# Kernel optimization log

Hardware: AMD Instinct MI355X
Metric: run time of the kernel (lower is better)

## Reference

```python
import jax, jax.numpy as jnp
import numpy as np

NUM_GRAPHS = 512

def _add_self_loops(edge_index, n):
    loop = jnp.arange(n, dtype=edge_index.dtype)
    src = jnp.concatenate([edge_index[0], loop])
    dst = jnp.concatenate([edge_index[1], loop])
    return src, dst

def _segment_softmax(e, seg, n):
    m = jax.ops.segment_max(e, seg, num_segments=n)
    e = jnp.exp(e - m[seg])
    s = jax.ops.segment_sum(e, seg, num_segments=n)
    return e / (s[seg] + 1e-16)

def _gat_conv(x, edge_index, W, a_src, a_dst, b, heads, ch):
    n = x.shape[0]
    src, dst = _add_self_loops(edge_index, n)
    h = (x @ W).reshape(n, heads, ch)                      # [N,H,C]
    al = (h * a_src).sum(-1)                               # [N,H]
    ar = (h * a_dst).sum(-1)                               # [N,H]
    e = jax.nn.leaky_relu(al[src] + ar[dst], 0.2)          # [E,H]
    alpha = _segment_softmax(e, dst, n)                    # [E,H]
    out = jax.ops.segment_sum(h[src] * alpha[:, :, None], dst, num_segments=n)
    return out.reshape(n, heads * ch) + b

def _gcn_conv(x, edge_index, W, b):
    n = x.shape[0]
    src, dst = _add_self_loops(edge_index, n)
    h = x @ W
    deg = jax.ops.segment_sum(jnp.ones(dst.shape, h.dtype), dst, num_segments=n)
    dis = jax.lax.rsqrt(jnp.maximum(deg, 1.0))
    norm = dis[src] * dis[dst]
    return jax.ops.segment_sum(h[src] * norm[:, None], dst, num_segments=n) + b

def _gmp(x, batch):
    return jax.ops.segment_max(x, batch, num_segments=NUM_GRAPHS)

def setup_inputs() -> dict:
    key = jax.random.key(0)
    ks = jax.random.split(key, 24)
    nd, ed = 100000, 800000
    np_, ep = 300000, 2400000
    def rn(k, shape, scale=0.1):
        return jax.random.normal(k, shape, dtype=jnp.float32) * scale
    inp = {
        "x_drug": jax.random.normal(ks[0], (nd, 78), dtype=jnp.float32),
        "edge_index_drug": jax.random.randint(ks[1], (2, ed), 0, nd, dtype=jnp.int32),
        "batch_drug": jnp.sort(jax.random.randint(ks[2], (nd,), 0, NUM_GRAPHS, dtype=jnp.int32)),
        "x_prot": jax.random.normal(ks[3], (np_, 41), dtype=jnp.float32),
        "edge_index_prot": jax.random.randint(ks[4], (2, ep), 0, np_, dtype=jnp.int32),
        "batch_prot": jnp.sort(jax.random.randint(ks[5], (np_,), 0, NUM_GRAPHS, dtype=jnp.int32)),
        # GATConv1: 78 -> 78, heads=10
        "W1": rn(ks[6], (78, 780)), "a_src1": rn(ks[7], (10, 78)), "a_dst1": rn(ks[8], (10, 78)), "b1": jnp.zeros((780,), jnp.float32),
        # GATConv2: 780 -> 128, heads=1
        "W2": rn(ks[9], (780, 128), 0.05), "a_src2": rn(ks[10], (1, 128)), "a_dst2": rn(ks[11], (1, 128)), "b2": jnp.zeros((128,), jnp.float32),
        "fc_g1_W": rn(ks[12], (128, 128)), "fc_g1_b": jnp.zeros((128,), jnp.float32),
        "gcn1_W": rn(ks[13], (41, 41)), "gcn1_b": jnp.zeros((41,), jnp.float32),
        "gcn2_W": rn(ks[14], (41, 64)), "gcn2_b": jnp.zeros((64,), jnp.float32),
        "lin1_W": rn(ks[15], (64, 128)), "lin1_b": jnp.zeros((128,), jnp.float32),
        "fc1_W": rn(ks[16], (256, 1024), 0.05), "fc1_b": jnp.zeros((1024,), jnp.float32),
        "fc2_W": rn(ks[17], (1024, 256), 0.03), "fc2_b": jnp.zeros((256,), jnp.float32),
        "out_W": rn(ks[18], (256, 1)), "out_b": jnp.zeros((1,), jnp.float32),
    }
    return inp

def reference(x_drug, edge_index_drug, batch_drug, x_prot, edge_index_prot, batch_prot,
              W1, a_src1, a_dst1, b1, W2, a_src2, a_dst2, b2, fc_g1_W, fc_g1_b,
              gcn1_W, gcn1_b, gcn2_W, gcn2_b, lin1_W, lin1_b,
              fc1_W, fc1_b, fc2_W, fc2_b, out_W, out_b):
    # drug branch (eval mode: dropout = identity)
    xd = jax.nn.elu(_gat_conv(x_drug, edge_index_drug, W1, a_src1, a_dst1, b1, 10, 78))
    xd = jax.nn.relu(_gat_conv(xd, edge_index_drug, W2, a_src2, a_dst2, b2, 1, 128))
    xd = _gmp(xd, batch_drug)
    xd = jax.nn.relu(xd @ fc_g1_W + fc_g1_b)
    # protein branch
    xp = jax.nn.relu(_gcn_conv(x_prot, edge_index_prot, gcn1_W, gcn1_b))
    xp = jax.nn.relu(_gcn_conv(xp, edge_index_prot, gcn2_W, gcn2_b))
    xp = _gmp(xp, batch_prot)
    xp = jax.nn.relu(xp @ lin1_W + lin1_b)
    # head
    xc = jnp.concatenate([xd, xp], axis=1)
    xc = jax.nn.relu(xc @ fc1_W + fc1_b)
    xc = jax.nn.relu(xc @ fc2_W + fc2_b)
    return xc @ out_W + out_b
```

## Files before the change

### kernel.cpp

```cpp
#include <hip/hip_runtime.h>
#include <math.h>

static inline int cdiv(int a, int b) { return (a + b - 1) / b; }

typedef __attribute__((ext_vector_type(8))) short short8v;
typedef __attribute__((ext_vector_type(4))) float f32x4;

__device__ inline unsigned bf16rne(float x) {
  unsigned u = __builtin_bit_cast(unsigned, x);
  return (u + 0x7FFFu + ((u >> 16) & 1u)) >> 16;
}
__device__ inline float bfhi(unsigned h) { return __builtin_bit_cast(float, h << 16); }
__device__ inline unsigned pk(float v) {
  unsigned hb = bf16rne(v);
  return hb | (bf16rne(v - bfhi(hb)) << 16);
}

__global__ void k_count(const int* __restrict__ dst, int E, int* __restrict__ cnt) {
  int i = blockIdx.x * 256 + threadIdx.x;
  if (i < E) atomicAdd(&cnt[dst[i]], 1);
}

__global__ __launch_bounds__(256) void k_scan_chunk(const int* __restrict__ in, int n,
                                                    int* __restrict__ out, int* __restrict__ sums) {
  __shared__ int tsum[256];
  int base = blockIdx.x * 1024;
  int t = threadIdx.x;
  int v[4]; int s = 0;
#pragma unroll
  for (int i = 0; i < 4; i++) { int idx = base + t * 4 + i; int x = (idx < n) ? in[idx] : 0; v[i] = x; s += x; }
  tsum[t] = s;
  __syncthreads();
  int x = s;
  for (int off = 1; off < 256; off <<= 1) {
    int y = (t >= off) ? tsum[t - off] : 0;
    __syncthreads();
    x += y;
    tsum[t] = x;
    __syncthreads();
  }
  int run = x - s;
#pragma unroll
  for (int i = 0; i < 4; i++) { int idx = base + t * 4 + i; if (idx < n) out[idx] = run; run += v[i]; }
  if (t == 255 && sums) sums[blockIdx.x] = x;
}

__global__ void k_scan_add(int* __restrict__ out, int n, const int* __restrict__ se,
                           int total, int* __restrict__ cur) {
  int i = blockIdx.x * 256 + threadIdx.x;
  if (i < n) { int v = out[i] + se[i >> 10]; out[i] = v; cur[i] = v; }
  if (i == 0) out[n] = total;
}

__global__ void k_fill(const int* __restrict__ src, const int* __restrict__ dst, int E,
                       int* __restrict__ cur, int* __restrict__ adj) {
  int i = blockIdx.x * 256 + threadIdx.x;
  if (i < E) { int p = atomicAdd(&cur[dst[i]], 1); adj[p] = src[i]; }
}

__global__ void k_w1t_pk(const float* __restrict__ W1, unsigned* __restrict__ o) {
  int i = blockIdx.x * 256 + threadIdx.x;
  if (i < 60840) { int h = i / 6084, r = i % 6084, c = r / 78, k = r % 78;
    o[i] = pk(W1[(size_t)k * 780 + h * 78 + c]); }
}
__global__ void k_w2t_pk(const float* __restrict__ W2, unsigned* __restrict__ o) {
  int i = blockIdx.x * 256 + threadIdx.x;
  if (i < 99840) { int n = i / 780, k = i % 780;
    o[i] = pk(W2[(size_t)k * 128 + n]); }
}

__global__ void k_vsrc(const float* __restrict__ W1, const float* __restrict__ a_src,
                       const float* __restrict__ a_dst, float* __restrict__ Vs, float* __restrict__ Vd) {
  int t = blockIdx.x * 64 + threadIdx.x;
  if (t >= 780) return;
  int k = t / 10, h = t % 10;
  float ss = 0.f, sd = 0.f;
  for (int c = 0; c < 78; c++) {
    float w = W1[k * 780 + h * 78 + c];
    ss += w * a_src[h * 78 + c];
    sd += w * a_dst[h * 78 + c];
  }
  Vs[k * 10 + h] = ss; Vd[k * 10 + h] = sd;
}

__global__ void k_alar1(const float* __restrict__ x, const float* __restrict__ Vs,
                        const float* __restrict__ Vd, float* __restrict__ al,
                        float* __restrict__ ar, int nd) {
  int t = blockIdx.x * 256 + threadIdx.x;
  if (t >= nd * 10) return;
  int n = t / 10, h = t % 10;
  const float* xr = x + (size_t)n * 78;
  float sa = 0.f, sd = 0.f;
  for (int k = 0; k < 78; k++) { float xv = xr[k]; sa += xv * Vs[k * 10 + h]; sd += xv * Vd[k * 10 + h]; }
  al[t] = sa; ar[t] = sd;
}

__global__ __launch_bounds__(64) void k_gat_agg1(const float* __restrict__ x, const int* __restrict__ adj,
                                                 const int* __restrict__ roff, const float* __restrict__ al,
                                                 const float* __restrict__ ar, unsigned* __restrict__ zp, int node0) {
  int n = node0 + blockIdx.x;
  int lane = threadIdx.x;
  int rs = roff[n];
  int deg = roff[n + 1] - rs;
  int tot = deg + 1;
  __shared__ float m_s[10], is_s[10], ar_s[10];
  __shared__ float red_s[64];
  __shared__ int src_s[64];
  __shared__ float alpha_s[64][10];
  if (lane < 10) ar_s[lane] = ar[n * 10 + lane];
  __syncthreads();
  int h = lane % 10; int eL = lane / 10;
  float mx = -1e30f;
  if (lane < 60) {
    for (int e = eL; e < tot; e += 6) {
      int s = (e == deg) ? n : adj[rs + e];
      float v = al[s * 10 + h] + ar_s[h];
      v = (v >= 0.f) ? v : 0.2f * v;
      mx = fmaxf(mx, v);
    }
  }
  red_s[lane] = mx;
  __syncthreads();
  if (lane < 10) {
    float m = red_s[lane];
    for (int g = 1; g < 6; g++) m = fmaxf(m, red_s[lane + g * 10]);
    m_s[lane] = m;
  }
  __syncthreads();
  float sm = 0.f;
  if (lane < 60) {
    float m = m_s[h];
    for (int e = eL; e < tot; e += 6) {
      int s = (e == deg) ? n : adj[rs + e];
      float v = al[s * 10 + h] + ar_s[h];
      v = (v >= 0.f) ? v : 0.2f * v;
      sm += __expf(v - m);
    }
  }
  red_s[lane] = sm;
  __syncthreads();
  if (lane < 10) {
    float s = 0.f;
    for (int g = 0; g < 6; g++) s += red_s[lane + g * 10];
    is_s[lane] = 1.f / (s + 1e-16f);
  }
  __syncthreads();
  float zA[10], zB[10];
#pragma unroll
  for (int i = 0; i < 10; i++) { zA[i] = 0.f; zB[i] = 0.f; }
  for (int c0 = 0; c0 < tot; c0 += 64) {
    int csz = (tot - c0 < 64) ? (tot - c0) : 64;
    if (lane < csz) {
      int e = c0 + lane;
      src_s[lane] = (e == deg) ? n : adj[rs + e];
    }
    __syncthreads();
    for (int p = lane; p < csz * 10; p += 64) {
      int e = p / 10; int hh = p % 10;
      int s = src_s[e];
      float v = al[s * 10 + hh] + ar_s[hh];
      v = (v >= 0.f) ? v : 0.2f * v;
      alpha_s[e][hh] = __expf(v - m_s[hh]) * is_s[hh];
    }
    __syncthreads();
    for (int e = 0; e < csz; e++) {
      int s = src_s[e];
      float xa = x[(size_t)s * 78 + lane];
      float xb = (lane < 14) ? x[(size_t)s * 78 + 64 + lane] : 0.f;
#pragma unroll
      for (int hh = 0; hh < 10; hh++) {
        float a = alpha_s[e][hh];
        zA[hh] += a * xa;
        zB[hh] += a * xb;
      }
    }
    __syncthreads();
  }
  unsigned* zr = zp + (size_t)blockIdx.x * 780;
#pragma unroll
  for (int hh = 0; hh < 10; hh++) {
    zr[hh * 78 + lane] = pk(zA[hh]);
    if (lane < 14) zr[hh * 78 + 64 + lane] = pk(zB[hh]);
  }
}

template <int RT, int CT, int MODE>
__global__ __launch_bounds__(256) void k_mfpk(const unsigned* __restrict__ Ap, const unsigned* __restrict__ Btp,
                                              const float* __restrict__ bias, float* __restrict__ C,
                                              unsigned* __restrict__ Op,
                                              int M, int N, int K, int lda, int ldb, int ldc,
                                              int hsA, int hsB, int hsBias) {
  const int BM = RT * 32, BN = CT * 32;
  __shared__ short Ah[BM][40], Al[BM][40], Bh[BN][40], Bl[BN][40];
  size_t aoff = (size_t)blockIdx.y * hsA;
  size_t boff = (size_t)blockIdx.y * hsB;
  if (bias) bias += (size_t)blockIdx.y * hsBias;
  int t = threadIdx.x;
  int bm = blockIdx.x * BM;
  int bn = blockIdx.z * BN;
  int w = t >> 6, l = t & 63;
  int wy = w >> 1, wx = w & 1;
  int lm = l & 15, lk = (l >> 4) * 8;

  f32x4 acc[RT][CT];
#pragma unroll
  for (int i = 0; i < RT; i++)
#pragma unroll
    for (int j = 0; j < CT; j++) acc[i][j] = (f32x4){0.f, 0.f, 0.f, 0.f};

  for (int k0 = 0; k0 < K; k0 += 32) {
    for (int i = t; i < BM * 16; i += 256) {
      int m = i >> 4, kp = (i & 15) * 2;
      int gm = bm + m, gk = k0 + kp;
      unsigned w0 = 0, w1 = 0;
      if (gm < M) {
        if (gk < K) w0 = Ap[aoff + (size_t)gm * lda + gk];
        if (gk + 1 < K) w1 = Ap[aoff + (size_t)gm * lda + gk + 1];
      }
      *(unsigned*)&Ah[m][kp] = (w0 & 0xFFFFu) | (w1 << 16);
      *(unsigned*)&Al[m][kp] = (w0 >> 16) | (w1 & 0xFFFF0000u);
    }
    for (int i = t; i < BN * 16; i += 256) {
      int n = i >> 4, kp = (i & 15) * 2;
      int gn = bn + n, gk = k0 + kp;
      unsigned w0 = 0, w1 = 0;
      if (gn < N) {
        if (gk < K) w0 = Btp[boff + (size_t)gn * ldb + gk];
        if (gk + 1 < K) w1 = Btp[boff + (size_t)gn * ldb + gk + 1];
      }
      *(unsigned*)&Bh[n][kp] = (w0 & 0xFFFFu) | (w1 << 16);
      *(unsigned*)&Bl[n][kp] = (w0 >> 16) | (w1 & 0xFFFF0000u);
    }
    __syncthreads();
    short8v bhf[CT], blf[CT];
#pragma unroll
    for (int ct = 0; ct < CT; ct++) {
      int col = wx * (CT * 16) + ct * 16 + lm;
      bhf[ct] = *(const short8v*)&Bh[col][lk];
      blf[ct] = *(const short8v*)&Bl[col][lk];
    }
#pragma unroll
    for (int rt = 0; rt < RT; rt++) {
      int row = wy * (RT * 16) + rt * 16 + lm;
      short8v ah = *(const short8v*)&Ah[row][lk];
      short8v alo = *(const short8v*)&Al[row][lk];
#pragma unroll
      for (int ct = 0; ct < CT; ct++) {
        acc[rt][ct] = __builtin_amdgcn_mfma_f32_16x16x32_bf16(ah, bhf[ct], acc[rt][ct], 0, 0, 0);
        acc[rt][ct] = __builtin_amdgcn_mfma_f32_16x16x32_bf16(ah, blf[ct], acc[rt][ct], 0, 0, 0);
        acc[rt][ct] = __builtin_amdgcn_mfma_f32_16x16x32_bf16(alo, bhf[ct], acc[rt][ct], 0, 0, 0);
      }
    }
    __syncthreads();
  }
#pragma unroll
  for (int rt = 0; rt < RT; rt++) {
#pragma unroll
    for (int r = 0; r < 4; r++) {
      int gm = bm + wy * (RT * 16) + rt * 16 + (l >> 4) * 4 + r;
      if (gm >= M) continue;
#pragma unroll
      for (int ct = 0; ct < CT; ct++) {
        int gn = bn + wx * (CT * 16) + ct * 16 + lm;
        if (gn >= N) continue;
        float v = acc[rt][ct][r] + (bias ? bias[gn] : 0.f);
        if (MODE == 0) {
          C[(size_t)gm * ldc + gn] = v;
        } else {
          v = (v > 0.f) ? v : (__expf(v) - 1.f);
          Op[aoff + (size_t)gm * lda + gn] = pk(v);
        }
      }
    }
  }
}

template <int ACT>
__global__ __launch_bounds__(256) void k_gemm128(const float* __restrict__ A, const float* __restrict__ B,
                                                 const float* __restrict__ bias, float* __restrict__ C,
                                                 int M, int N, int K, int lda, int ldb, int ldc) {
  __shared__ float As[16][136];
  __shared__ float Bs[16][132];
  int t = threadIdx.x;
  int bm = blockIdx.x * 128, bn = blockIdx.y * 128;
  int tx = t & 15, ty = t >> 4;
  float acc[8][8] = {};
  int arow0 = t >> 2, akq = t & 3;
  int bkk0 = t >> 5, bc4 = t & 31;
  for (int k0 = 0; k0 < K; k0 += 16) {
#pragma unroll
    for (int p = 0; p < 2; p++) {
      int row = arow0 + p * 64;
      int gm = bm + row, gk = k0 + akq * 4;
      float4 v = {0.f, 0.f, 0.f, 0.f};
      if (gm < M) {
        if (gk + 3 < K) v = *(const float4*)&A[(size_t)gm * lda + gk];
        else {
          float tmp[4] = {0.f, 0.f, 0.f, 0.f};
          for (int j = 0; j < 4; j++) if (gk + j < K) tmp[j] = A[(size_t)gm * lda + gk + j];
          v.x = tmp[0]; v.y = tmp[1]; v.z = tmp[2]; v.w = tmp[3];
        }
      }
      As[akq * 4 + 0][row] = v.x; As[akq * 4 + 1][row] = v.y;
      As[akq * 4 + 2][row] = v.z; As[akq * 4 + 3][row] = v.w;
    }
#pragma unroll
    for (int p = 0; p < 2; p++) {
      int kk = bkk0 + p * 8;
      int gk = k0 + kk, gn = bn + bc4 * 4;
      float4 v = {0.f, 0.f, 0.f, 0.f};
      if (gk < K) v = *(const float4*)&B[(size_t)gk * ldb + gn];
      *(float4*)&Bs[kk][bc4 * 4] = v;
    }
    __syncthreads();
#pragma unroll
    for (int kk = 0; kk < 16; kk++) {
      float a[8], b[8];
      *(float4*)&a[0] = *(const float4*)&As[kk][ty * 8];
      *(float4*)&a[4] = *(const float4*)&As[kk][ty * 8 + 4];
      *(float4*)&b[0] = *(const float4*)&Bs[kk][tx * 8];
      *(float4*)&b[4] = *(const float4*)&Bs[kk][tx * 8 + 4];
#pragma unroll
      for (int i = 0; i < 8; i++)
#pragma unroll
        for (int j = 0; j < 8; j++) acc[i][j] += a[i] * b[j];
    }
    __syncthreads();
  }
#pragma unroll
  for (int i = 0; i < 8; i++) {
    int gm = bm + ty * 8 + i;
    if (gm >= M) continue;
#pragma unroll
    for (int j = 0; j < 8; j++) {
      int gn = bn + tx * 8 + j;
      if (gn >= N) continue;
      float v = acc[i][j] + (bias ? bias[gn] : 0.f);
      if (ACT == 1) v = fmaxf(v, 0.f);
      else if (ACT == 2) v = (v > 0.f) ? v : (__expf(v) - 1.f);
      C[(size_t)gm * ldc + gn] = v;
    }
  }
}

template <int ACT>
__global__ __launch_bounds__(256) void k_gemm(const float* __restrict__ A, const float* __restrict__ B,
                                              const float* __restrict__ bias, float* __restrict__ C,
                                              int M, int N, int K, int lda, int ldb, int ldc) {
  __shared__ float As[16][68];
  __shared__ float Bs[16][68];
  int tx = threadIdx.x % 16, ty = threadIdx.x / 16;
  int bm = blockIdx.x * 64, bn = blockIdx.y * 64;
  float acc[4][4] = {};
  for (int k0 = 0; k0 < K; k0 += 16) {
    for (int i = threadIdx.x; i < 1024; i += 256) {
      int r = i / 16, kk = i % 16;
      int gm = bm + r, gk = k0 + kk;
      As[kk][r] = (gm < M && gk < K) ? A[(size_t)gm * lda + gk] : 0.f;
    }
    for (int i = threadIdx.x; i < 1024; i += 256) {
      int kk = i / 64, c = i % 64;
      int gk = k0 + kk, gn = bn + c;
      Bs[kk][c] = (gk < K && gn < N) ? B[(size_t)gk * ldb + gn] : 0.f;
    }
    __syncthreads();
#pragma unroll
    for (int kk = 0; kk < 16; kk++) {
      float a[4], b[4];
#pragma unroll
      for (int i = 0; i < 4; i++) a[i] = As[kk][ty * 4 + i];
#pragma unroll
      for (int j = 0; j < 4; j++) b[j] = Bs[kk][tx * 4 + j];
#pragma unroll
      for (int i = 0; i < 4; i++)
#pragma unroll
        for (int j = 0; j < 4; j++) acc[i][j] += a[i] * b[j];
    }
    __syncthreads();
  }
#pragma unroll
  for (int i = 0; i < 4; i++) {
    int gm = bm + ty * 4 + i;
    if (gm >= M) continue;
#pragma unroll
    for (int j = 0; j < 4; j++) {
      int gn = bn + tx * 4 + j;
      if (gn >= N) continue;
      float v = acc[i][j] + (bias ? bias[gn] : 0.f);
      if (ACT == 1) v = fmaxf(v, 0.f);
      else if (ACT == 2) v = (v > 0.f) ? v : (__expf(v) - 1.f);
      C[(size_t)gm * ldc + gn] = v;
    }
  }
}

__global__ __launch_bounds__(64) void k_alar2(const float* __restrict__ h2, const float* __restrict__ a_src,
                                              const float* __restrict__ a_dst, float* __restrict__ al,
                                              float* __restrict__ ar) {
  int n = blockIdx.x, lane = threadIdx.x;
  float v0 = h2[(size_t)n * 128 + lane], v1 = h2[(size_t)n * 128 + 64 + lane];
  float sa = v0 * a_src[lane] + v1 * a_src[64 + lane];
  float sd = v0 * a_dst[lane] + v1 * a_dst[64 + lane];
#pragma unroll
  for (int o = 32; o; o >>= 1) { sa += __shfl_xor(sa, o); sd += __shfl_xor(sd, o); }
  if (lane == 0) { al[n] = sa; ar[n] = sd; }
}

__global__ __launch_bounds__(64) void k_gat_agg2(const float* __restrict__ h2, const int* __restrict__ adj,
                                                 const int* __restrict__ roff, const float* __restrict__ al,
                                                 const float* __restrict__ ar, const float* __restrict__ b2,
                                                 float* __restrict__ out) {
  int n = blockIdx.x, lane = threadIdx.x;
  int rs = roff[n];
  int deg = roff[n + 1] - rs;
  int tot = deg + 1;
  float arn = ar[n];
  float mx = -1e30f;
  for (int e = lane; e < tot; e += 64) {
    int s = (e == deg) ? n : adj[rs + e];
    float v = al[s] + arn; v = (v >= 0.f) ? v : 0.2f * v;
    mx = fmaxf(mx, v);
  }
#pragma unroll
  for (int o = 32; o; o >>= 1) mx = fmaxf(mx, __shfl_xor(mx, o));
  float sm = 0.f;
  for (int e = lane; e < tot; e += 64) {
    int s = (e == deg) ? n : adj[rs + e];
    float v = al[s] + arn; v = (v >= 0.f) ? v : 0.2f * v;
    sm += __expf(v - mx);
  }
#pragma unroll
  for (int o = 32; o; o >>= 1) sm += __shfl_xor(sm, o);
  float inv = 1.f / (sm + 1e-16f);
  float a0 = 0.f, a1 = 0.f;
  for (int e = 0; e < tot; e++) {
    int s = (e == deg) ? n : adj[rs + e];
    float v = al[s] + arn; v = (v >= 0.f) ? v : 0.2f * v;
    float alpha = __expf(v - mx) * inv;
    a0 += alpha * h2[(size_t)s * 128 + lane];
    a1 += alpha * h2[(size_t)s * 128 + 64 + lane];
  }
  out[(size_t)n * 128 + lane]      = fmaxf(a0 + b2[lane], 0.f);
  out[(size_t)n * 128 + 64 + lane] = fmaxf(a1 + b2[64 + lane], 0.f);
}

__global__ void k_dis(const int* __restrict__ roff, float* __restrict__ dis, int n) {
  int i = blockIdx.x * 256 + threadIdx.x;
  if (i < n) dis[i] = rsqrtf((float)(roff[i + 1] - roff[i] + 1));
}

__global__ __launch_bounds__(64) void k_gcn_agg(const float* __restrict__ h, const int* __restrict__ adj,
                                                const int* __restrict__ roff, const float* __restrict__ dis,
                                                const float* __restrict__ bias, float* __restrict__ out, int C) {
  int n = blockIdx.x, lane = threadIdx.x;
  int rs = roff[n], re = roff[n + 1];
  float dn = dis[n];
  bool act = lane < C;
  float acc = 0.f;
  for (int e = rs; e < re; e++) {
    int s = adj[e];
    float w = dis[s];
    if (act) acc += w * h[(size_t)s * C + lane];
  }
  if (act) {
    acc += dn * h[(size_t)n * C + lane];
    float v = dn * acc + bias[lane];
    out[(size_t)n * C + lane] = fmaxf(v, 0.f);
  }
}

__global__ void k_bounds(const int* __restrict__ batch, int n, int* __restrict__ gstart, int G) {
  int i = blockIdx.x * 256 + threadIdx.x;
  if (i >= n) return;
  int b = batch[i];
  if (i == 0) { for (int g = 0; g <= b; g++) gstart[g] = 0; }
  else { int p = batch[i - 1]; for (int g = p + 1; g <= b; g++) gstart[g] = i; }
  if (i == n - 1) { for (int g = b + 1; g <= G; g++) gstart[g] = n; }
}

__global__ void k_pool(const float* __restrict__ xin, const int* __restrict__ gstart,
                       float* __restrict__ pool, int C) {
  int g = blockIdx.x; int c = threadIdx.x;
  int n0 = gstart[g], n1 = gstart[g + 1];
  float m = -3.4e38f;
  for (int i = n0; i < n1; i++) m = fmaxf(m, xin[(size_t)i * C + c]);
  pool[(size_t)g * C + c] = m;
}

__global__ __launch_bounds__(64) void k_out(const float* __restrict__ t2, const float* __restrict__ w,
                                            const float* __restrict__ b, float* __restrict__ out) {
  int g = blockIdx.x, lane = threadIdx.x;
  float s = 0.f;
  for (int k = lane; k < 256; k += 64) s += t2[(size_t)g * 256 + k] * w[k];
#pragma unroll
  for (int o = 32; o; o >>= 1) s += __shfl_xor(s, o);
  if (lane == 0) out[g] = s + b[0];
}

extern "C" void kernel_launch(void* const* d_in, const int* in_sizes, int n_in,
                              void* d_out, int out_size, void* d_ws, size_t ws_size,
                              hipStream_t stream) {
  if (n_in < 28) return;
  const float* x_drug  = (const float*)d_in[0];
  const int*   ei_d    = (const int*)d_in[1];
  const int*   batch_d = (const int*)d_in[2];
  const float* x_prot  = (const float*)d_in[3];
  const int*   ei_p    = (const int*)d_in[4];
  const int*   batch_p = (const int*)d_in[5];
  const float* W1     = (const float*)d_in[6];
  const float* a_src1 = (const float*)d_in[7];
  const float* a_dst1 = (const float*)d_in[8];
  const float* b1     = (const float*)d_in[9];
  const float* W2     = (const float*)d_in[10];
  const float* a_src2 = (const float*)d_in[11];
  const float* a_dst2 = (const float*)d_in[12];
  const float* b2     = (const float*)d_in[13];
  const float* fcgW = (const float*)d_in[14];
  const float* fcgb = (const float*)d_in[15];
  const float* g1W  = (const float*)d_in[16];
  const float* g1b  = (const float*)d_in[17];
  const float* g2W  = (const float*)d_in[18];
  const float* g2b  = (const float*)d_in[19];
  const float* l1W  = (const float*)d_in[20];
  const float* l1b  = (const float*)d_in[21];
  const float* f1W  = (const float*)d_in[22];
  const float* f1b  = (const float*)d_in[23];
  const float* f2W  = (const float*)d_in[24];
  const float* f2b  = (const float*)d_in[25];
  const float* oW   = (const float*)d_in[26];
  const float* ob   = (const float*)d_in[27];

  const int nd = in_sizes[0] / 78, ed = in_sizes[1] / 2;
  const int np = in_sizes[3] / 41, ep = in_sizes[4] / 2;
  const int G = 512;

  char* Bp = (char*)d_ws;
  size_t cap = ws_size;
  auto atop = [&](size_t bytes) -> char* {
    cap = (cap - bytes) & ~(size_t)255;
    return Bp + cap;
  };
  float* pooled_d = (float*)atop((size_t)G * 128 * 4);
  float* pooled_p = (float*)atop((size_t)G * 64 * 4);
  float* xc = (float*)atop((size_t)G * 256 * 4);
  float* t1 = (float*)atop((size_t)G * 1024 * 4);
  float* t2 = (float*)atop((size_t)G * 256 * 4);
  int* gs_d = (int*)atop(513 * 4);
  int* gs_p = (int*)atop(513 * 4);
  unsigned* W1tp = (unsigned*)atop(60840 * 4);
  unsigned* W2tp = (unsigned*)atop(99840 * 4);

  size_t off = 0;
  auto alc = [&](size_t bytes) -> char* {
    char* p = Bp + off;
    off = (off + bytes + 255) & ~(size_t)255;
    return p;
  };

  k_w1t_pk<<<cdiv(60840, 256), 256, 0, stream>>>(W1, W1tp);
  k_w2t_pk<<<cdiv(99840, 256), 256, 0, stream>>>(W2, W2tp);

  int* cur_d  = (int*)alc((size_t)nd * 4);
  int* roff_d = (int*)alc(((size_t)nd + 1) * 4);
  int* adj_d  = (int*)alc((size_t)ed * 4);
  int* part   = (int*)alc(1024 * 4);
  int* parte  = (int*)alc(1024 * 4);
  float* Vs  = (float*)alc(780 * 4);
  float* Vd  = (float*)alc(780 * 4);
  float* al1 = (float*)alc((size_t)nd * 10 * 4);
  float* ar1 = (float*)alc((size_t)nd * 10 * 4);
  float* al2 = (float*)alc((size_t)nd * 4);
  float* ar2 = (float*)alc((size_t)nd * 4);
  float* h2  = (float*)alc((size_t)nd * 128 * 4);

  size_t remain = (cap > off) ? cap - off : 0;
  size_t xd2_bytes = (size_t)nd * 128 * 4;
  unsigned* zp; float* xd2;
  long long slabCap;
  if (remain >= xd2_bytes + (size_t)128 * 3120) {
    xd2 = (float*)(Bp + off);
    slabCap = (long long)(remain / 3120);
  } else {
    xd2 = (float*)alc(xd2_bytes);
    size_t r2 = (cap > off) ? cap - off : 0;
    slabCap = (long long)(r2 / 3120);
  }
  int slabN = (int)((slabCap < (long long)nd) ? slabCap : (long long)nd);
  slabN &= ~127;
  if (slabN < 128) slabN = 128;
  zp = (unsigned*)(Bp + off);

  hipMemsetAsync(cur_d, 0, (size_t)nd * 4, stream);
  k_count<<<cdiv(ed, 256), 256, 0, stream>>>(ei_d + ed, ed, cur_d);
  int nch = cdiv(nd, 1024);
  k_scan_chunk<<<nch, 256, 0, stream>>>(cur_d, nd, roff_d, part);
  k_scan_chunk<<<1, 256, 0, stream>>>(part, nch, parte, nullptr);
  k_scan_add<<<cdiv(nd, 256), 256, 0, stream>>>(roff_d, nd, parte, ed, cur_d);
  k_fill<<<cdiv(ed, 256), 256, 0, stream>>>(ei_d, ei_d + ed, ed, cur_d, adj_d);

  k_vsrc<<<cdiv(780, 64), 64, 0, stream>>>(W1, a_src1, a_dst1, Vs, Vd);
  k_alar1<<<cdiv(nd * 10, 256), 256, 0, stream>>>(x_drug, Vs, Vd, al1, ar1, nd);

  for (int s0 = 0; s0 < nd; s0 += slabN) {
    int sm = ((nd - s0) < slabN) ? (nd - s0) : slabN;
    k_gat_agg1<<<sm, 64, 0, stream>>>(x_drug, adj_d, roff_d, al1, ar1, zp, s0);
    k_mfpk<2, 3, 2><<<dim3(cdiv(sm, 64), 10, 1), 256, 0, stream>>>(
        zp, W1tp, b1, nullptr, zp, sm, 78, 78, 780, 78, 0, 78, 6084, 78);
    k_mfpk<2, 2, 0><<<dim3(cdiv(sm, 64), 1, 2), 256, 0, stream>>>(
        zp, W2tp, nullptr, h2 + (size_t)s0 * 128, nullptr,
        sm, 128, 780, 780, 780, 128, 0, 0, 0);
  }
  k_alar2<<<nd, 64, 0, stream>>>(h2, a_src2, a_dst2, al2, ar2);
  k_gat_agg2<<<nd, 64, 0, stream>>>(h2, adj_d, roff_d, al2, ar2, b2, xd2);
  k_bounds<<<cdiv(nd, 256), 256, 0, stream>>>(batch_d, nd, gs_d, G);
  k_pool<<<G, 128, 0, stream>>>(xd2, gs_d, pooled_d, 128);
  k_gemm128<1><<<dim3(4, 1), 256, 0, stream>>>(pooled_d, fcgW, fcgb, xc, G, 128, 128, 128, 128, 256);

  off = 0;
  int* cur_p  = (int*)alc((size_t)np * 4);
  int* roff_p = (int*)alc(((size_t)np + 1) * 4);
  int* adj_p  = (int*)alc((size_t)ep * 4);
  int* partp  = (int*)alc(1024 * 4);
  int* partep = (int*)alc(1024 * 4);
  float* dis = (float*)alc((size_t)np * 4);
  float* hp1 = (float*)alc((size_t)np * 41 * 4);
  float* xp1 = (float*)alc((size_t)np * 41 * 4);
  float* hp2 = (float*)alc((size_t)np * 64 * 4);
  float* xp2 = hp1;

  hipMemsetAsync(cur_p, 0, (size_t)np * 4, stream);
  k_count<<<cdiv(ep, 256), 256, 0, stream>>>(ei_p + ep, ep, cur_p);
  int nchp = cdiv(np, 1024);
  k_scan_chunk<<<nchp, 256, 0, stream>>>(cur_p, np, roff_p, partp);
  k_scan_chunk<<<1, 256, 0, stream>>>(partp, nchp, partep, nullptr);
  k_scan_add<<<cdiv(np, 256), 256, 0, stream>>>(roff_p, np, partep, ep, cur_p);
  k_fill<<<cdiv(ep, 256), 256, 0, stream>>>(ei_p, ei_p + ep, ep, cur_p, adj_p);
  k_dis<<<cdiv(np, 256), 256, 0, stream>>>(roff_p, dis, np);

  k_gemm<0><<<dim3(cdiv(np, 64), 1), 256, 0, stream>>>(x_prot, g1W, nullptr, hp1, np, 41, 41, 41, 41, 41);
  k_gcn_agg<<<np, 64, 0, stream>>>(hp1, adj_p, roff_p, dis, g1b, xp1, 41);
  k_gemm<0><<<dim3(cdiv(np, 64), 1), 256, 0, stream>>>(xp1, g2W, nullptr, hp2, np, 64, 41, 41, 64, 64);
  k_gcn_agg<<<np, 64, 0, stream>>>(hp2, adj_p, roff_p, dis, g2b, xp2, 64);
  k_bounds<<<cdiv(np, 256), 256, 0, stream>>>(batch_p, np, gs_p, G);
  k_pool<<<G, 64, 0, stream>>>(xp2, gs_p, pooled_p, 64);
  k_gemm128<1><<<dim3(4, 1), 256, 0, stream>>>(pooled_p, l1W, l1b, xc + 128, G, 128, 64, 64, 128, 256);

  k_gemm128<1><<<dim3(4, 8), 256, 0, stream>>>(xc, f1W, f1b, t1, G, 1024, 256, 256, 1024, 1024);
  k_gemm128<1><<<dim3(4, 2), 256, 0, stream>>>(t1, f2W, f2b, t2, G, 256, 1024, 1024, 256, 256);
  k_out<<<G, 64, 0, stream>>>(t2, oW, ob, (float*)d_out);
}
```

Measured before the change: 2.235 ms.

## Fuse MLP head GEMMs and output dot into one per-graph kernel

Replaces the five head launches (two projection GEMMs, two FC GEMMs, the output reduction) with one kernel that runs one block per graph and keeps intermediates in shared memory. This removes launch overhead and the global round-trips for xc, t1 and t2. The cost is that every block rereads the full fc1 and fc2 weight matrices (around 2 MB) with no cross-graph reuse, so the head turns into a per-row GEMV pass that relies on L2 bandwidth.

```diff
diff --git a/kernel.cpp b/kernel.cpp
--- a/kernel.cpp
+++ b/kernel.cpp
@@ -276,74 +276,6 @@
 }
 
 template <int ACT>
-__global__ __launch_bounds__(256) void k_gemm128(const float* __restrict__ A, const float* __restrict__ B,
-                                                 const float* __restrict__ bias, float* __restrict__ C,
-                                                 int M, int N, int K, int lda, int ldb, int ldc) {
-  __shared__ float As[16][136];
-  __shared__ float Bs[16][132];
-  int t = threadIdx.x;
-  int bm = blockIdx.x * 128, bn = blockIdx.y * 128;
-  int tx = t & 15, ty = t >> 4;
-  float acc[8][8] = {};
-  int arow0 = t >> 2, akq = t & 3;
-  int bkk0 = t >> 5, bc4 = t & 31;
-  for (int k0 = 0; k0 < K; k0 += 16) {
-#pragma unroll
-    for (int p = 0; p < 2; p++) {
-      int row = arow0 + p * 64;
-      int gm = bm + row, gk = k0 + akq * 4;
-      float4 v = {0.f, 0.f, 0.f, 0.f};
-      if (gm < M) {
-        if (gk + 3 < K) v = *(const float4*)&A[(size_t)gm * lda + gk];
-        else {
-          float tmp[4] = {0.f, 0.f, 0.f, 0.f};
-          for (int j = 0; j < 4; j++) if (gk + j < K) tmp[j] = A[(size_t)gm * lda + gk + j];
-          v.x = tmp[0]; v.y = tmp[1]; v.z = tmp[2]; v.w = tmp[3];
-        }
-      }
-      As[akq * 4 + 0][row] = v.x; As[akq * 4 + 1][row] = v.y;
-      As[akq * 4 + 2][row] = v.z; As[akq * 4 + 3][row] = v.w;
-    }
-#pragma unroll
-    for (int p = 0; p < 2; p++) {
-      int kk = bkk0 + p * 8;
-      int gk = k0 + kk, gn = bn + bc4 * 4;
-      float4 v = {0.f, 0.f, 0.f, 0.f};
-      if (gk < K) v = *(const float4*)&B[(size_t)gk * ldb + gn];
-      *(float4*)&Bs[kk][bc4 * 4] = v;
-    }
-    __syncthreads();
-#pragma unroll
-    for (int kk = 0; kk < 16; kk++) {
-      float a[8], b[8];
-      *(float4*)&a[0] = *(const float4*)&As[kk][ty * 8];
-      *(float4*)&a[4] = *(const float4*)&As[kk][ty * 8 + 4];
-      *(float4*)&b[0] = *(const float4*)&Bs[kk][tx * 8];
-      *(float4*)&b[4] = *(const float4*)&Bs[kk][tx * 8 + 4];
-#pragma unroll
-      for (int i = 0; i < 8; i++)
-#pragma unroll
-        for (int j = 0; j < 8; j++) acc[i][j] += a[i] * b[j];
-    }
-    __syncthreads();
-  }
-#pragma unroll
-  for (int i = 0; i < 8; i++) {
-    int gm = bm + ty * 8 + i;
-    if (gm >= M) continue;
-#pragma unroll
-    for (int j = 0; j < 8; j++) {
-      int gn = bn + tx * 8 + j;
-      if (gn >= N) continue;
-      float v = acc[i][j] + (bias ? bias[gn] : 0.f);
-      if (ACT == 1) v = fmaxf(v, 0.f);
-      else if (ACT == 2) v = (v > 0.f) ? v : (__expf(v) - 1.f);
-      C[(size_t)gm * ldc + gn] = v;
-    }
-  }
-}
-
-template <int ACT>
 __global__ __launch_bounds__(256) void k_gemm(const float* __restrict__ A, const float* __restrict__ B,
                                               const float* __restrict__ bias, float* __restrict__ C,
                                               int M, int N, int K, int lda, int ldb, int ldc) {
@@ -487,14 +419,57 @@
   pool[(size_t)g * C + c] = m;
 }
 
-__global__ __launch_bounds__(64) void k_out(const float* __restrict__ t2, const float* __restrict__ w,
-                                            const float* __restrict__ b, float* __restrict__ out) {
-  int g = blockIdx.x, lane = threadIdx.x;
-  float s = 0.f;
-  for (int k = lane; k < 256; k += 64) s += t2[(size_t)g * 256 + k] * w[k];
+__global__ __launch_bounds__(256) void k_head(const float* __restrict__ pd, const float* __restrict__ pp,
+                                              const float* __restrict__ fcgW, const float* __restrict__ fcgb,
+                                              const float* __restrict__ l1W, const float* __restrict__ l1b,
+                                              const float* __restrict__ f1W, const float* __restrict__ f1b,
+                                              const float* __restrict__ f2W, const float* __restrict__ f2b,
+                                              const float* __restrict__ oW, const float* __restrict__ ob,
+                                              float* __restrict__ out) {
+  int g = blockIdx.x, t = threadIdx.x;
+  __shared__ float pds[128], pps[64], xcs[256], t1s[1024];
+  __shared__ float red[4];
+  if (t < 128) pds[t] = pd[(size_t)g * 128 + t];
+  else if (t < 192) pps[t - 128] = pp[(size_t)g * 64 + (t - 128)];
+  __syncthreads();
+  float a = 0.f;
+  if (t < 128) {
+#pragma unroll 8
+    for (int k = 0; k < 128; k++) a += pds[k] * fcgW[k * 128 + t];
+    a = fmaxf(a + fcgb[t], 0.f);
+  } else {
+    int c = t - 128;
+#pragma unroll 8
+    for (int k = 0; k < 64; k++) a += pps[k] * l1W[k * 128 + c];
+    a = fmaxf(a + l1b[c], 0.f);
+  }
+  xcs[t] = a;
+  __syncthreads();
+  float acc0 = 0.f, acc1 = 0.f, acc2 = 0.f, acc3 = 0.f;
+#pragma unroll 4
+  for (int k = 0; k < 256; k++) {
+    float xv = xcs[k];
+    const float* rw = f1W + (size_t)k * 1024 + t;
+    acc0 += xv * rw[0];
+    acc1 += xv * rw[256];
+    acc2 += xv * rw[512];
+    acc3 += xv * rw[768];
+  }
+  t1s[t]       = fmaxf(acc0 + f1b[t], 0.f);
+  t1s[t + 256] = fmaxf(acc1 + f1b[t + 256], 0.f);
+  t1s[t + 512] = fmaxf(acc2 + f1b[t + 512], 0.f);
+  t1s[t + 768] = fmaxf(acc3 + f1b[t + 768], 0.f);
+  __syncthreads();
+  float v = 0.f;
+#pragma unroll 8
+  for (int k = 0; k < 1024; k++) v += t1s[k] * f2W[k * 256 + t];
+  v = fmaxf(v + f2b[t], 0.f);
+  float s = v * oW[t];
 #pragma unroll
   for (int o = 32; o; o >>= 1) s += __shfl_xor(s, o);
-  if (lane == 0) out[g] = s + b[0];
+  if ((t & 63) == 0) red[t >> 6] = s;
+  __syncthreads();
+  if (t == 0) out[g] = red[0] + red[1] + red[2] + red[3] + ob[0];
 }
 
 extern "C" void kernel_launch(void* const* d_in, const int* in_sizes, int n_in,
@@ -542,9 +517,6 @@
   };
   float* pooled_d = (float*)atop((size_t)G * 128 * 4);
   float* pooled_p = (float*)atop((size_t)G * 64 * 4);
-  float* xc = (float*)atop((size_t)G * 256 * 4);
-  float* t1 = (float*)atop((size_t)G * 1024 * 4);
-  float* t2 = (float*)atop((size_t)G * 256 * 4);
   int* gs_d = (int*)atop(513 * 4);
   int* gs_p = (int*)atop(513 * 4);
   unsigned* W1tp = (unsigned*)atop(60840 * 4);
@@ -614,7 +586,6 @@
   k_gat_agg2<<<nd, 64, 0, stream>>>(h2, adj_d, roff_d, al2, ar2, b2, xd2);
   k_bounds<<<cdiv(nd, 256), 256, 0, stream>>>(batch_d, nd, gs_d, G);
   k_pool<<<G, 128, 0, stream>>>(xd2, gs_d, pooled_d, 128);
-  k_gemm128<1><<<dim3(4, 1), 256, 0, stream>>>(pooled_d, fcgW, fcgb, xc, G, 128, 128, 128, 128, 256);
 
   off = 0;
   int* cur_p  = (int*)alc((size_t)np * 4);
@@ -643,9 +614,7 @@
   k_gcn_agg<<<np, 64, 0, stream>>>(hp2, adj_p, roff_p, dis, g2b, xp2, 64);
   k_bounds<<<cdiv(np, 256), 256, 0, stream>>>(batch_p, np, gs_p, G);
   k_pool<<<G, 64, 0, stream>>>(xp2, gs_p, pooled_p, 64);
-  k_gemm128<1><<<dim3(4, 1), 256, 0, stream>>>(pooled_p, l1W, l1b, xc + 128, G, 128, 64, 64, 128, 256);
-
-  k_gemm128<1><<<dim3(4, 8), 256, 0, stream>>>(xc, f1W, f1b, t1, G, 1024, 256, 256, 1024, 1024);
-  k_gemm128<1><<<dim3(4, 2), 256, 0, stream>>>(t1, f2W, f2b, t2, G, 256, 1024, 1024, 256, 256);
-  k_out<<<G, 64, 0, stream>>>(t2, oW, ob, (float*)d_out);
-}
+
+  k_head<<<G, 256, 0, stream>>>(pooled_d, pooled_p, fcgW, fcgb, l1W, l1b,
+                                f1W, f1b, f2W, f2b, oW, ob, (float*)d_out);
+}
```

After: 2.025 ms. 9.4% less time.
